# Optimization experiments

Measured on AMD Instinct MI355X. Metric: run time of the kernel, lower is better.

The kernel has to match this reference:

```python
import jax, jax.numpy as jnp
import numpy as np

N_USERS = 50000
N_ITEMS = 30000
N_ENTITIES = 100000
N_RELATIONS = 50
N_EDGES = 1500000
N_INTER = 1000000
D = 64
GAMMA = 0.1
MAX_ITER = 3


def _seg_sum(x, idx, n):
    return jax.ops.segment_sum(x, idx, num_segments=n)


def _seg_mean(x, idx, n):
    s = _seg_sum(x, idx, n)
    c = _seg_sum(jnp.ones((x.shape[0], 1), x.dtype), idx, n)
    return s / jnp.clip(c, 1.0)


def _masked_seg_mean(x, mask, idx, n):
    # scatter_mean over the subset of rows where mask is True (zeros for empty segments)
    w = mask.astype(x.dtype)[:, None]
    s = _seg_sum(x * w, idx, n)
    c = _seg_sum(w, idx, n)
    return s / jnp.clip(c, 1.0)


def _seg_softmax(p, idx, n):
    m = jax.ops.segment_max(p, idx, num_segments=n)
    e = jnp.exp(p - m[idx])
    z = _seg_sum(e, idx, n)
    return e / z[idx]


def _leaky_relu(x):
    return jnp.where(x >= 0, x, 0.01 * x)


def _normalize(x, eps=1e-12):
    n = jnp.linalg.norm(x, axis=1, keepdims=True)
    return x / jnp.maximum(n, eps)


def setup_inputs() -> dict:
    key = jax.random.key(0)
    ks = jax.random.split(key, 12)
    entity_emb = jax.random.normal(ks[0], (N_ENTITIES, D), jnp.float32) * 0.1
    user_emb = jax.random.normal(ks[1], (N_USERS, D), jnp.float32) * 0.1
    user_emb_cf = jax.random.normal(ks[2], (N_USERS, D), jnp.float32) * 0.1
    item_emb_cf = jax.random.normal(ks[3], (N_ITEMS, D), jnp.float32) * 0.1
    relation_weight = jax.random.normal(ks[4], (N_RELATIONS, D), jnp.float32) * 0.1
    edge_index = jax.random.randint(ks[5], (2, N_EDGES), 0, N_ENTITIES, jnp.int64 if jax.config.jax_enable_x64 else jnp.int32)
    edge_type = jax.random.randint(ks[6], (N_EDGES,), 0, N_RELATIONS, edge_index.dtype)
    rows = jax.random.randint(ks[7], (N_INTER, 1), 0, N_USERS, edge_index.dtype)
    cols = jax.random.randint(ks[8], (N_INTER, 1), 0, N_ITEMS, edge_index.dtype)
    interact_mat = jnp.concatenate([rows, cols], axis=1)
    W1_w = jax.random.normal(ks[9], (D, D), jnp.float32) * 0.1
    W1_b = jnp.zeros((D,), jnp.float32)
    W2_w = jax.random.normal(ks[10], (D, D), jnp.float32) * 0.1
    W2_b = jnp.zeros((D,), jnp.float32)
    return {
        "entity_emb": entity_emb, "user_emb": user_emb, "user_emb_cf": user_emb_cf,
        "item_emb_cf": item_emb_cf, "relation_weight": relation_weight,
        "W1_w": W1_w, "W1_b": W1_b, "W2_w": W2_w, "W2_b": W2_b,
        "edge_index": edge_index, "edge_type": edge_type, "interact_mat": interact_mat,
    }


def reference(entity_emb, user_emb, user_emb_cf, item_emb_cf, relation_weight,
              W1_w, W1_b, W2_w, W2_b, edge_index, edge_type, interact_mat):
    head, tail = edge_index[0], edge_index[1]
    cross = (head < N_ITEMS) ^ (tail < N_ITEMS)
    same = ~cross

    rel_emb = relation_weight[edge_type]          # [E, D]
    tail_emb = entity_emb[tail]                   # [E, D]

    agg1 = _masked_seg_mean(tail_emb * rel_emb, cross, head, N_ENTITIES)
    agg1 = _leaky_relu(agg1 @ W1_w.T + W1_b) / 2
    agg2 = _masked_seg_mean(tail_emb + rel_emb, same, head, N_ENTITIES)
    agg2 = _leaky_relu(agg2 @ W2_w.T + W2_b) / 2
    entity_agg = agg1 + agg2
    rel_ = _seg_mean(rel_emb, head, N_ENTITIES)   # [n_entities, D]

    mat_row = interact_mat[:, 0]
    mat_col = interact_mat[:, 1]
    item_emb_kg = entity_emb[:N_ITEMS]
    rel_i = rel_[:N_ITEMS]

    u, ucf, mask = None, None, None
    for i in range(MAX_ITER):
        ue = user_emb if u is None else u
        ucfe = user_emb_cf if ucf is None else ucf
        p = jax.nn.sigmoid(jnp.sum(ue[mat_row] * rel_i[mat_col] * item_emb_kg[mat_col], axis=1))
        pcf = jax.nn.sigmoid(jnp.sum(ucfe[mat_row] * item_emb_cf[mat_col], axis=1))
        p = _seg_softmax(p, mat_row, N_USERS)
        pcf = _seg_softmax(pcf, mat_row, N_USERS)
        mask = (jnp.abs(jax.nn.sigmoid(p) - jax.nn.sigmoid(pcf)) < GAMMA).astype(jnp.int32)[:, None]
        mf = mask.astype(p.dtype)
        u = _seg_sum(item_emb_kg[mat_col] * p[:, None] * mf, mat_row, N_USERS)
        ucf = _seg_sum(item_emb_cf[mat_col] * pcf[:, None] * mf, mat_row, N_USERS)
        if i < MAX_ITER - 1:
            u = _normalize(u)
            ucf = _normalize(ucf)

    item_agg = _seg_mean(user_emb_cf[mat_row], mat_col, N_ITEMS)
    return entity_agg, u, ucf, item_agg, mask
```

## Files before the change

kernel.cpp:

```cpp
#include <hip/hip_runtime.h>

#define NU 50000
#define NI 30000
#define NE 100000
#define NEDGE 1500000
#define NINTER 1000000
#define GAMMA 0.1f
#define CAP 192
#define KR 5
#define KSTG (4 * KR)
#define SB 1024

#define STRIPE_E 12500
#define STRIPE_R 6250
#define STRIPE_C 3750
#define SCATB 2048

__device__ __forceinline__ float frcp(float x) { return __builtin_amdgcn_rcpf(x); }
__device__ __forceinline__ float fsgm(float x) { return frcp(1.0f + __expf(-x)); }
__device__ __forceinline__ float dot4(float4 a, float4 b) {
  return a.x * b.x + a.y * b.y + a.z * b.z + a.w * b.w;
}
__device__ __forceinline__ int gidx(const void* p, long long i, int is64) {
  return is64 ? (int)((const long long*)p)[i] : ((const int*)p)[i];
}

__global__ void k_detect(const int* __restrict__ ei32, int* __restrict__ flag) {
  int all_zero = 1;
  for (int i = 1; i < 64; i += 2)
    if (ei32[i] != 0) { all_zero = 0; break; }
  *flag = all_zero;
}

__global__ __launch_bounds__(256) void k_hist(
    const void* __restrict__ ei, const void* __restrict__ im,
    int* __restrict__ cntE, int* __restrict__ cntR,
    int* __restrict__ cntC, const int* __restrict__ flagp) {
  int f = *flagp;
  int coh = blockIdx.x & 7;
  int ct = (blockIdx.x >> 3) * 256 + threadIdx.x;
  int cstride = (gridDim.x >> 3) * 256;
  int loE = coh * STRIPE_E, hiE = loE + STRIPE_E;
  int loR = coh * STRIPE_R, hiR = loR + STRIPE_R;
  int loC = coh * STRIPE_C, hiC = loC + STRIPE_C;
  for (int e = ct; e < NEDGE; e += cstride) {
    int h = gidx(ei, e, f);
    if (h >= loE && h < hiE) atomicAdd(&cntE[h], 1);
  }
  for (int t = ct; t < NINTER; t += cstride) {
    int r = gidx(im, 2LL * t, f);
    int c = gidx(im, 2LL * t + 1, f);
    if (r >= loR && r < hiR) atomicAdd(&cntR[r], 1);
    if (c >= loC && c < hiC) atomicAdd(&cntC[c], 1);
  }
}

__global__ void k_scan1(const int* __restrict__ in, int* __restrict__ out,
                        int* __restrict__ part, int n) {
  __shared__ int tmp[SB];
  int g = blockIdx.x * SB + threadIdx.x;
  int v = (g < n) ? in[g] : 0;
  tmp[threadIdx.x] = v; __syncthreads();
  for (int off = 1; off < SB; off <<= 1) {
    int t = (threadIdx.x >= off) ? tmp[threadIdx.x - off] : 0;
    __syncthreads();
    tmp[threadIdx.x] += t;
    __syncthreads();
  }
  if (g < n) out[g] = tmp[threadIdx.x] - v;
  if (threadIdx.x == SB - 1) part[blockIdx.x] = tmp[threadIdx.x];
}

__global__ void k_scan2(int* __restrict__ part, int nb) {
  __shared__ int tmp[SB];
  int v = (threadIdx.x < nb) ? part[threadIdx.x] : 0;
  tmp[threadIdx.x] = v; __syncthreads();
  for (int off = 1; off < SB; off <<= 1) {
    int t = (threadIdx.x >= off) ? tmp[threadIdx.x - off] : 0;
    __syncthreads();
    tmp[threadIdx.x] += t;
    __syncthreads();
  }
  if (threadIdx.x < nb) part[threadIdx.x] = tmp[threadIdx.x] - v;
}

__global__ void k_scan3(int* __restrict__ out, const int* __restrict__ part, int n) {
  int g = blockIdx.x * SB + threadIdx.x;
  if (g < n) out[g] += part[blockIdx.x];
}

__global__ __launch_bounds__(256) void k_scat(
    const void* __restrict__ ei, const void* __restrict__ et,
    const void* __restrict__ im,
    const int* __restrict__ startE, int* __restrict__ curE, int* __restrict__ SE,
    const int* __restrict__ startR, int* __restrict__ curR,
    int* __restrict__ SIcol, int* __restrict__ SIorig,
    const int* __restrict__ startC, int* __restrict__ curC,
    int* __restrict__ SCrow, const int* __restrict__ flagp) {
  int f = *flagp;
  int coh = blockIdx.x & 7;
  int ct = (blockIdx.x >> 3) * 256 + threadIdx.x;
  int cstride = (gridDim.x >> 3) * 256;
  int loE = coh * STRIPE_E, hiE = loE + STRIPE_E;
  int loR = coh * STRIPE_R, hiR = loR + STRIPE_R;
  int loC = coh * STRIPE_C, hiC = loC + STRIPE_C;
  for (int e = ct; e < NEDGE; e += cstride) {
    int h = gidx(ei, e, f);
    if (h >= loE && h < hiE) {
      int tl = gidx(ei, NEDGE + (long long)e, f), r = gidx(et, e, f);
      int pos = startE[h] + atomicAdd(&curE[h], 1);
      SE[pos] = tl | (r << 17);
    }
  }
  for (int t = ct; t < NINTER; t += cstride) {
    int r = gidx(im, 2LL * t, f);
    int c = gidx(im, 2LL * t + 1, f);
    if (r >= loR && r < hiR) {
      int pr = startR[r] + atomicAdd(&curR[r], 1);
      SIcol[pr] = c; SIorig[pr] = t;
    }
    if (c >= loC && c < hiC) {
      int pc = startC[c] + atomicAdd(&curC[c], 1);
      SCrow[pc] = r;
    }
  }
}

__global__ __launch_bounds__(256) void k_aggE(
    const int* __restrict__ SE, const int* __restrict__ startE, const int* __restrict__ cntE,
    const float* __restrict__ ent, const float* __restrict__ relw,
    const float* __restrict__ W1w, const float* __restrict__ W1b,
    const float* __restrict__ W2w, const float* __restrict__ W2b,
    float* __restrict__ out_entity, float* __restrict__ RIE) {
  __shared__ float w1[64 * 65], w2[64 * 65], b1[64], b2[64];
  __shared__ float xs1[4][64], xs2[4][64], xs3[4][64];
  int tid = threadIdx.x;
  for (int i = tid; i < 4096; i += 256) {
    w1[(i >> 6) * 65 + (i & 63)] = W1w[i];
    w2[(i >> 6) * 65 + (i & 63)] = W2w[i];
  }
  if (tid < 64) { b1[tid] = W1b[tid]; b2[tid] = W2b[tid]; }
  __syncthreads();
  int w = tid >> 6, lane = tid & 63;
  int g = lane >> 4, q = lane & 15;
  int h = blockIdx.x * 4 + w;
  if (h >= NE) return;
  int s = startE[h], n = cntE[h];
  bool hI = (h < NI);
  float4 a1 = {0, 0, 0, 0}, a2 = {0, 0, 0, 0}, rs = {0, 0, 0, 0};
  int c1 = 0;
  for (int i0 = 0; i0 < n; i0 += 4) {
    int i = i0 + g;
    bool act = i < n;
    if (act) {
      int v = SE[s + i];
      int tl = v & 0x1FFFF, rl = v >> 17;
      const float4 te = *(const float4*)&ent[tl * 64 + 4 * q];
      const float4 re = *(const float4*)&relw[rl * 64 + 4 * q];
      rs.x += re.x; rs.y += re.y; rs.z += re.z; rs.w += re.w;
      if (hI != (tl < NI)) {
        a1.x += te.x * re.x; a1.y += te.y * re.y;
        a1.z += te.z * re.z; a1.w += te.w * re.w;
        c1++;
      } else {
        a2.x += te.x + re.x; a2.y += te.y + re.y;
        a2.z += te.z + re.z; a2.w += te.w + re.w;
      }
    }
  }
#pragma unroll
  for (int off = 16; off <= 32; off <<= 1) {
    a1.x += __shfl_xor(a1.x, off, 64); a1.y += __shfl_xor(a1.y, off, 64);
    a1.z += __shfl_xor(a1.z, off, 64); a1.w += __shfl_xor(a1.w, off, 64);
    a2.x += __shfl_xor(a2.x, off, 64); a2.y += __shfl_xor(a2.y, off, 64);
    a2.z += __shfl_xor(a2.z, off, 64); a2.w += __shfl_xor(a2.w, off, 64);
    rs.x += __shfl_xor(rs.x, off, 64); rs.y += __shfl_xor(rs.y, off, 64);
    rs.z += __shfl_xor(rs.z, off, 64); rs.w += __shfl_xor(rs.w, off, 64);
    c1 += __shfl_xor(c1, off, 64);
  }
  int c2 = n - c1;
  float r1 = frcp((float)max(c1, 1)), r2 = frcp((float)max(c2, 1));
  float rn = frcp((float)max(n, 1));
  if (g == 0) {
    *(float4*)&xs1[w][4 * q] = make_float4(a1.x * r1, a1.y * r1, a1.z * r1, a1.w * r1);
    *(float4*)&xs2[w][4 * q] = make_float4(a2.x * r2, a2.y * r2, a2.z * r2, a2.w * r2);
    *(float4*)&xs3[w][4 * q] = make_float4(rs.x * rn, rs.y * rn, rs.z * rn, rs.w * rn);
  }
  __asm__ volatile("s_waitcnt lgkmcnt(0)");
  int d = lane;
  float acc1 = b1[d], acc2 = b2[d];
#pragma unroll 8
  for (int k = 0; k < 64; k++) {
    acc1 += xs1[w][k] * w1[d * 65 + k];
    acc2 += xs2[w][k] * w2[d * 65 + k];
  }
  acc1 = (acc1 >= 0.f ? acc1 : 0.01f * acc1) * 0.5f;
  acc2 = (acc2 >= 0.f ? acc2 : 0.01f * acc2) * 0.5f;
  out_entity[h * 64 + d] = acc1 + acc2;
  if (hI) RIE[h * 64 + d] = xs3[w][d] * ent[h * 64 + d];
}

__global__ __launch_bounds__(256, 4) void k_phaseB(
    const int* __restrict__ SIcol, const int* __restrict__ SIorig,
    const int* __restrict__ startR, const int* __restrict__ cntR,
    const float* __restrict__ ue, const float* __restrict__ uce,
    const float* __restrict__ RIE, const float* __restrict__ ent,
    const float* __restrict__ icf,
    float* __restrict__ out_u, float* __restrict__ out_ucf,
    float* __restrict__ out_mask) {
  __shared__ float eP[4][CAP + 4], ePC[4][CAP + 4];
  __shared__ int cols[4][CAP + 4];
  int tid = threadIdx.x, w = tid >> 6, lane = tid & 63;
  int g = lane >> 4, q = lane & 15;
  int r = blockIdx.x * 4 + w;
  if (r >= NU) return;
  int s = startR[r], n = cntR[r];
  if (n > CAP) n = CAP;
  for (int i = lane; i < n; i += 64) cols[w][i] = SIcol[s + i];
  __asm__ volatile("s_waitcnt lgkmcnt(0) vmcnt(0)");
  float4 u4  = *(const float4*)&ue[r * 64 + 4 * q];
  float4 uc4 = *(const float4*)&uce[r * 64 + 4 * q];

  float4 rieS[KR], icfS[KR], entS[KR];
#pragma unroll
  for (int kk = 0; kk < KR; kk++) {
    int i = 4 * kk + g;
    rieS[kk] = make_float4(0, 0, 0, 0);
    icfS[kk] = make_float4(0, 0, 0, 0);
    entS[kk] = make_float4(0, 0, 0, 0);
    if (i < n) {
      int c = cols[w][i];
      rieS[kk] = *(const float4*)&RIE[c * 64 + 4 * q];
      icfS[kk] = *(const float4*)&icf[c * 64 + 4 * q];
      entS[kk] = *(const float4*)&ent[c * 64 + 4 * q];
    }
  }

  for (int it = 0; it < 3; it++) {
    float Zp = 0.f, ZCp = 0.f;
    float epS[KR], epcS[KR];
#pragma unroll
    for (int kk = 0; kk < KR; kk++) {
      int i = 4 * kk + g;
      bool act = i < n;
      float v1 = 0.f, v2 = 0.f;
      if (act) {
        v1 = dot4(u4,  rieS[kk]);
        v2 = dot4(uc4, icfS[kk]);
      }
#pragma unroll
      for (int off = 1; off <= 8; off <<= 1) {
        v1 += __shfl_xor(v1, off, 64);
        v2 += __shfl_xor(v2, off, 64);
      }
      float ep = __expf(fsgm(v1)), epc = __expf(fsgm(v2));
      epS[kk] = ep; epcS[kk] = epc;
      if (act) { Zp += ep; ZCp += epc; }
    }
    for (int i0 = KSTG; i0 < n; i0 += 4) {
      int i = i0 + g;
      bool act = i < n;
      float v1 = 0.f, v2 = 0.f;
      if (act) {
        int c = cols[w][i];
        v1 = dot4(u4,  *(const float4*)&RIE[c * 64 + 4 * q]);
        v2 = dot4(uc4, *(const float4*)&icf[c * 64 + 4 * q]);
      }
#pragma unroll
      for (int off = 1; off <= 8; off <<= 1) {
        v1 += __shfl_xor(v1, off, 64);
        v2 += __shfl_xor(v2, off, 64);
      }
      float ep = __expf(fsgm(v1)), epc = __expf(fsgm(v2));
      if (act) {
        if (q == 0) { eP[w][i] = ep; ePC[w][i] = epc; }
        Zp += ep; ZCp += epc;
      }
    }
    float Zs = Zp, ZCs = ZCp;
#pragma unroll
    for (int off = 16; off <= 32; off <<= 1) {
      Zs += __shfl_xor(Zs, off, 64);
      ZCs += __shfl_xor(ZCs, off, 64);
    }
    __asm__ volatile("s_waitcnt lgkmcnt(0)");
    float rz = frcp(Zs), rzc = frcp(ZCs);
    float4 ua = {0, 0, 0, 0}, uca = {0, 0, 0, 0};
#pragma unroll
    for (int kk = 0; kk < KR; kk++) {
      int i = 4 * kk + g;
      if (i < n) {
        float p = epS[kk] * rz, pc = epcS[kk] * rzc;
        bool m = fabsf(fsgm(p) - fsgm(pc)) < GAMMA;
        if (it == 2 && q == 0) out_mask[SIorig[s + i]] = m ? 1.0f : 0.0f;
        if (m) {
          ua.x += entS[kk].x * p; ua.y += entS[kk].y * p;
          ua.z += entS[kk].z * p; ua.w += entS[kk].w * p;
          uca.x += icfS[kk].x * pc; uca.y += icfS[kk].y * pc;
          uca.z += icfS[kk].z * pc; uca.w += icfS[kk].w * pc;
        }
      }
    }
    for (int i0 = KSTG; i0 < n; i0 += 4) {
      int i = i0 + g;
      if (i < n) {
        int c = cols[w][i];
        float p = eP[w][i] * rz, pc = ePC[w][i] * rzc;
        bool m = fabsf(fsgm(p) - fsgm(pc)) < GAMMA;
        if (it == 2 && q == 0) out_mask[SIorig[s + i]] = m ? 1.0f : 0.0f;
        if (m) {
          const float4 e4 = *(const float4*)&ent[c * 64 + 4 * q];
          const float4 i4 = *(const float4*)&icf[c * 64 + 4 * q];
          ua.x += e4.x * p; ua.y += e4.y * p; ua.z += e4.z * p; ua.w += e4.w * p;
          uca.x += i4.x * pc; uca.y += i4.y * pc; uca.z += i4.z * pc; uca.w += i4.w * pc;
        }
      }
    }
#pragma unroll
    for (int off = 16; off <= 32; off <<= 1) {
      ua.x += __shfl_xor(ua.x, off, 64); ua.y += __shfl_xor(ua.y, off, 64);
      ua.z += __shfl_xor(ua.z, off, 64); ua.w += __shfl_xor(ua.w, off, 64);
      uca.x += __shfl_xor(uca.x, off, 64); uca.y += __shfl_xor(uca.y, off, 64);
      uca.z += __shfl_xor(uca.z, off, 64); uca.w += __shfl_xor(uca.w, off, 64);
    }
    if (it < 2) {
      float s1 = dot4(ua, ua), s2 = dot4(uca, uca);
#pragma unroll
      for (int off = 1; off <= 8; off <<= 1) {
        s1 += __shfl_xor(s1, off, 64);
        s2 += __shfl_xor(s2, off, 64);
      }
      float k1 = frcp(fmaxf(sqrtf(s1), 1e-12f)), k2 = frcp(fmaxf(sqrtf(s2), 1e-12f));
      ua.x *= k1; ua.y *= k1; ua.z *= k1; ua.w *= k1;
      uca.x *= k2; uca.y *= k2; uca.z *= k2; uca.w *= k2;
    }
    u4 = ua; uc4 = uca;
  }
  if (g == 0) {
    *(float4*)&out_u[r * 64 + 4 * q] = u4;
    *(float4*)&out_ucf[r * 64 + 4 * q] = uc4;
  }
}

__global__ __launch_bounds__(256) void k_itemA(
    const int* __restrict__ SCrow, const int* __restrict__ startC,
    const int* __restrict__ cntC, const float* __restrict__ ucf,
    float* __restrict__ out_item) {
  int tid = threadIdx.x, w = tid >> 6, lane = tid & 63;
  int g = lane >> 4, q = lane & 15;
  int c = blockIdx.x * 4 + w;
  if (c >= NI) return;
  int s = startC[c], n = cntC[c];
  float4 a = {0, 0, 0, 0};
  for (int i0 = 0; i0 < n; i0 += 4) {
    int i = i0 + g;
    if (i < n) {
      const float4 v = *(const float4*)&ucf[SCrow[s + i] * 64 + 4 * q];
      a.x += v.x; a.y += v.y; a.z += v.z; a.w += v.w;
    }
  }
#pragma unroll
  for (int off = 16; off <= 32; off <<= 1) {
    a.x += __shfl_xor(a.x, off, 64); a.y += __shfl_xor(a.y, off, 64);
    a.z += __shfl_xor(a.z, off, 64); a.w += __shfl_xor(a.w, off, 64);
  }
  float rn = frcp((float)max(n, 1));
  if (g == 0) {
    *(float4*)&out_item[c * 64 + 4 * q] =
        make_float4(a.x * rn, a.y * rn, a.z * rn, a.w * rn);
  }
}

static void scan(int* cnt, int* start, int* part, int n, hipStream_t st) {
  int nb = (n + SB - 1) / SB;
  k_scan1<<<nb, SB, 0, st>>>(cnt, start, part, n);
  k_scan2<<<1, SB, 0, st>>>(part, nb);
  k_scan3<<<nb, SB, 0, st>>>(start, part, n);
}

extern "C" void kernel_launch(void* const* d_in, const int* in_sizes, int n_in,
                              void* d_out, int out_size, void* d_ws, size_t ws_size,
                              hipStream_t stream) {
  const float* entity_emb  = (const float*)d_in[0];
  const float* user_emb    = (const float*)d_in[1];
  const float* user_emb_cf = (const float*)d_in[2];
  const float* item_emb_cf = (const float*)d_in[3];
  const float* relw        = (const float*)d_in[4];
  const float* W1w = (const float*)d_in[5];
  const float* W1b = (const float*)d_in[6];
  const float* W2w = (const float*)d_in[7];
  const float* W2b = (const float*)d_in[8];
  const void* edge_index   = d_in[9];
  const void* edge_type    = d_in[10];
  const void* interact_mat = d_in[11];

  float* out = (float*)d_out;
  float* out_entity = out;
  float* out_u      = out + 6400000;
  float* out_ucf    = out + 9600000;
  float* out_item   = out + 12800000;
  float* out_mask   = out + 14720000;

  float* W = (float*)d_ws;
  int*   SE     = (int*)W;
  int*   SIcol  = (int*)(W + 3000000);
  int*   SIorig = (int*)(W + 4000000);
  int*   SCrow  = (int*)(W + 5000000);
  float* RIE    = W + 6000000;
  int*   cntE   = (int*)(W + 7920000);
  int*   startE = (int*)(W + 8020000);
  int*   curE   = (int*)(W + 8120000);
  int*   cntR   = (int*)(W + 8220000);
  int*   startR = (int*)(W + 8270000);
  int*   curR   = (int*)(W + 8320000);
  int*   cntC   = (int*)(W + 8370000);
  int*   startC = (int*)(W + 8400000);
  int*   curC   = (int*)(W + 8430000);
  int*   part   = (int*)(W + 8460000);
  int*   FL     = (int*)(W + 8462048);

  k_detect<<<1, 1, 0, stream>>>((const int*)edge_index, FL);
  hipMemsetAsync(cntE, 0, (size_t)(8462048 - 7920000) * 4, stream);

  k_hist<<<SCATB, 256, 0, stream>>>(edge_index, interact_mat, cntE, cntR, cntC, FL);
  scan(cntE, startE, part, NE, stream);
  scan(cntR, startR, part, NU, stream);
  scan(cntC, startC, part, NI, stream);
  k_scat<<<SCATB, 256, 0, stream>>>(edge_index, edge_type, interact_mat,
                                    startE, curE, SE,
                                    startR, curR, SIcol, SIorig,
                                    startC, curC, SCrow, FL);

  k_aggE<<<(NE + 3) / 4, 256, 0, stream>>>(SE, startE, cntE, entity_emb, relw,
                                           W1w, W1b, W2w, W2b, out_entity, RIE);
  k_phaseB<<<(NU + 3) / 4, 256, 0, stream>>>(SIcol, SIorig, startR, cntR,
                                             user_emb, user_emb_cf, RIE,
                                             entity_emb, item_emb_cf,
                                             out_u, out_ucf, out_mask);
  k_itemA<<<(NI + 3) / 4, 256, 0, stream>>>(SCrow, startC, cntC, user_emb_cf, out_item);
}
```

Measured before the change: 900.8 us.

## Merge scans, pretranspose MLP weights, use DPP reductions, raise phaseB occupancy

Several independent changes. The three CSR prefix scans become one scan over a concatenated count array, with per-segment bias subtraction, which cuts kernel launches. k_aggE drops its per-block shared-memory weight staging and reads pre-transposed weights from global/L2 so consecutive lanes read coalesced addresses. k_phaseB swaps shfl_xor reductions for DPP row reductions, keeps entity rows and exp scores in LDS rather than registers, and raises launch bounds to 8 waves per SIMD, trading more LDS per block for lower register pressure.

```diff
diff --git a/kernel.cpp b/kernel.cpp
--- a/kernel.cpp
+++ b/kernel.cpp
@@ -10,6 +10,7 @@
 #define KR 5
 #define KSTG (4 * KR)
 #define SB 1024
+#define NSCAN 180000
 
 #define STRIPE_E 12500
 #define STRIPE_R 6250
@@ -23,6 +24,14 @@
 }
 __device__ __forceinline__ int gidx(const void* p, long long i, int is64) {
   return is64 ? (int)((const long long*)p)[i] : ((const int*)p)[i];
+}
+
+__device__ __forceinline__ float red16(float v) {
+  v += __int_as_float(__builtin_amdgcn_update_dpp(0, __float_as_int(v), 0xB1, 0xF, 0xF, true));
+  v += __int_as_float(__builtin_amdgcn_update_dpp(0, __float_as_int(v), 0x4E, 0xF, 0xF, true));
+  v += __int_as_float(__builtin_amdgcn_update_dpp(0, __float_as_int(v), 0x141, 0xF, 0xF, true));
+  v += __int_as_float(__builtin_amdgcn_update_dpp(0, __float_as_int(v), 0x140, 0xF, 0xF, true));
+  return v;
 }
 
 __global__ void k_detect(const int* __restrict__ ei32, int* __restrict__ flag) {
@@ -30,6 +39,16 @@
   for (int i = 1; i < 64; i += 2)
     if (ei32[i] != 0) { all_zero = 0; break; }
   *flag = all_zero;
+}
+
+__global__ void k_wt(const float* __restrict__ W1w, const float* __restrict__ W2w,
+                     float* __restrict__ WT1, float* __restrict__ WT2) {
+  int i = blockIdx.x * 256 + threadIdx.x;
+  if (i < 4096) {
+    int r = i >> 6, c = i & 63;
+    WT1[c * 64 + r] = W1w[i];
+    WT2[c * 64 + r] = W2w[i];
+  }
 }
 
 __global__ __launch_bounds__(256) void k_hist(
@@ -86,7 +105,10 @@
 
 __global__ void k_scan3(int* __restrict__ out, const int* __restrict__ part, int n) {
   int g = blockIdx.x * SB + threadIdx.x;
-  if (g < n) out[g] += part[blockIdx.x];
+  if (g < n) {
+    int bias = (g >= 150000) ? (NEDGE + NINTER) : ((g >= 100000) ? NEDGE : 0);
+    out[g] += part[blockIdx.x] - bias;
+  }
 }
 
 __global__ __launch_bounds__(256) void k_scat(
@@ -129,18 +151,11 @@
 __global__ __launch_bounds__(256) void k_aggE(
     const int* __restrict__ SE, const int* __restrict__ startE, const int* __restrict__ cntE,
     const float* __restrict__ ent, const float* __restrict__ relw,
-    const float* __restrict__ W1w, const float* __restrict__ W1b,
-    const float* __restrict__ W2w, const float* __restrict__ W2b,
+    const float* __restrict__ WT1, const float* __restrict__ W1b,
+    const float* __restrict__ WT2, const float* __restrict__ W2b,
     float* __restrict__ out_entity, float* __restrict__ RIE) {
-  __shared__ float w1[64 * 65], w2[64 * 65], b1[64], b2[64];
   __shared__ float xs1[4][64], xs2[4][64], xs3[4][64];
   int tid = threadIdx.x;
-  for (int i = tid; i < 4096; i += 256) {
-    w1[(i >> 6) * 65 + (i & 63)] = W1w[i];
-    w2[(i >> 6) * 65 + (i & 63)] = W2w[i];
-  }
-  if (tid < 64) { b1[tid] = W1b[tid]; b2[tid] = W2b[tid]; }
-  __syncthreads();
   int w = tid >> 6, lane = tid & 63;
   int g = lane >> 4, q = lane & 15;
   int h = blockIdx.x * 4 + w;
@@ -188,11 +203,11 @@
   }
   __asm__ volatile("s_waitcnt lgkmcnt(0)");
   int d = lane;
-  float acc1 = b1[d], acc2 = b2[d];
+  float acc1 = W1b[d], acc2 = W2b[d];
 #pragma unroll 8
   for (int k = 0; k < 64; k++) {
-    acc1 += xs1[w][k] * w1[d * 65 + k];
-    acc2 += xs2[w][k] * w2[d * 65 + k];
+    acc1 += xs1[w][k] * WT1[k * 64 + d];
+    acc2 += xs2[w][k] * WT2[k * 64 + d];
   }
   acc1 = (acc1 >= 0.f ? acc1 : 0.01f * acc1) * 0.5f;
   acc2 = (acc2 >= 0.f ? acc2 : 0.01f * acc2) * 0.5f;
@@ -200,7 +215,7 @@
   if (hI) RIE[h * 64 + d] = xs3[w][d] * ent[h * 64 + d];
 }
 
-__global__ __launch_bounds__(256, 4) void k_phaseB(
+__global__ __launch_bounds__(256, 8) void k_phaseB(
     const int* __restrict__ SIcol, const int* __restrict__ SIorig,
     const int* __restrict__ startR, const int* __restrict__ cntR,
     const float* __restrict__ ue, const float* __restrict__ uce,
@@ -210,6 +225,7 @@
     float* __restrict__ out_mask) {
   __shared__ float eP[4][CAP + 4], ePC[4][CAP + 4];
   __shared__ int cols[4][CAP + 4];
+  __shared__ float entL[4][KSTG][68];
   int tid = threadIdx.x, w = tid >> 6, lane = tid & 63;
   int g = lane >> 4, q = lane & 15;
   int r = blockIdx.x * 4 + w;
@@ -221,24 +237,22 @@
   float4 u4  = *(const float4*)&ue[r * 64 + 4 * q];
   float4 uc4 = *(const float4*)&uce[r * 64 + 4 * q];
 
-  float4 rieS[KR], icfS[KR], entS[KR];
+  float4 rieS[KR], icfS[KR];
 #pragma unroll
   for (int kk = 0; kk < KR; kk++) {
     int i = 4 * kk + g;
     rieS[kk] = make_float4(0, 0, 0, 0);
     icfS[kk] = make_float4(0, 0, 0, 0);
-    entS[kk] = make_float4(0, 0, 0, 0);
     if (i < n) {
       int c = cols[w][i];
       rieS[kk] = *(const float4*)&RIE[c * 64 + 4 * q];
       icfS[kk] = *(const float4*)&icf[c * 64 + 4 * q];
-      entS[kk] = *(const float4*)&ent[c * 64 + 4 * q];
+      *(float4*)&entL[w][i][4 * q] = *(const float4*)&ent[c * 64 + 4 * q];
     }
   }
 
   for (int it = 0; it < 3; it++) {
     float Zp = 0.f, ZCp = 0.f;
-    float epS[KR], epcS[KR];
 #pragma unroll
     for (int kk = 0; kk < KR; kk++) {
       int i = 4 * kk + g;
@@ -248,14 +262,12 @@
         v1 = dot4(u4,  rieS[kk]);
         v2 = dot4(uc4, icfS[kk]);
       }
-#pragma unroll
-      for (int off = 1; off <= 8; off <<= 1) {
-        v1 += __shfl_xor(v1, off, 64);
-        v2 += __shfl_xor(v2, off, 64);
-      }
+      v1 = red16(v1); v2 = red16(v2);
       float ep = __expf(fsgm(v1)), epc = __expf(fsgm(v2));
-      epS[kk] = ep; epcS[kk] = epc;
-      if (act) { Zp += ep; ZCp += epc; }
+      if (act) {
+        if (q == 0) { eP[w][i] = ep; ePC[w][i] = epc; }
+        Zp += ep; ZCp += epc;
+      }
     }
     for (int i0 = KSTG; i0 < n; i0 += 4) {
       int i = i0 + g;
@@ -266,11 +278,7 @@
         v1 = dot4(u4,  *(const float4*)&RIE[c * 64 + 4 * q]);
         v2 = dot4(uc4, *(const float4*)&icf[c * 64 + 4 * q]);
       }
-#pragma unroll
-      for (int off = 1; off <= 8; off <<= 1) {
-        v1 += __shfl_xor(v1, off, 64);
-        v2 += __shfl_xor(v2, off, 64);
-      }
+      v1 = red16(v1); v2 = red16(v2);
       float ep = __expf(fsgm(v1)), epc = __expf(fsgm(v2));
       if (act) {
         if (q == 0) { eP[w][i] = ep; ePC[w][i] = epc; }
@@ -290,12 +298,12 @@
     for (int kk = 0; kk < KR; kk++) {
       int i = 4 * kk + g;
       if (i < n) {
-        float p = epS[kk] * rz, pc = epcS[kk] * rzc;
+        float p = eP[w][i] * rz, pc = ePC[w][i] * rzc;
         bool m = fabsf(fsgm(p) - fsgm(pc)) < GAMMA;
         if (it == 2 && q == 0) out_mask[SIorig[s + i]] = m ? 1.0f : 0.0f;
         if (m) {
-          ua.x += entS[kk].x * p; ua.y += entS[kk].y * p;
-          ua.z += entS[kk].z * p; ua.w += entS[kk].w * p;
+          const float4 e4 = *(const float4*)&entL[w][i][4 * q];
+          ua.x += e4.x * p; ua.y += e4.y * p; ua.z += e4.z * p; ua.w += e4.w * p;
           uca.x += icfS[kk].x * pc; uca.y += icfS[kk].y * pc;
           uca.z += icfS[kk].z * pc; uca.w += icfS[kk].w * pc;
         }
@@ -324,12 +332,8 @@
       uca.z += __shfl_xor(uca.z, off, 64); uca.w += __shfl_xor(uca.w, off, 64);
     }
     if (it < 2) {
-      float s1 = dot4(ua, ua), s2 = dot4(uca, uca);
-#pragma unroll
-      for (int off = 1; off <= 8; off <<= 1) {
-        s1 += __shfl_xor(s1, off, 64);
-        s2 += __shfl_xor(s2, off, 64);
-      }
+      float s1 = red16(dot4(ua, ua));
+      float s2 = red16(dot4(uca, uca));
       float k1 = frcp(fmaxf(sqrtf(s1), 1e-12f)), k2 = frcp(fmaxf(sqrtf(s2), 1e-12f));
       ua.x *= k1; ua.y *= k1; ua.z *= k1; ua.w *= k1;
       uca.x *= k2; uca.y *= k2; uca.z *= k2; uca.w *= k2;
@@ -371,13 +375,6 @@
   }
 }
 
-static void scan(int* cnt, int* start, int* part, int n, hipStream_t st) {
-  int nb = (n + SB - 1) / SB;
-  k_scan1<<<nb, SB, 0, st>>>(cnt, start, part, n);
-  k_scan2<<<1, SB, 0, st>>>(part, nb);
-  k_scan3<<<nb, SB, 0, st>>>(start, part, n);
-}
-
 extern "C" void kernel_launch(void* const* d_in, const int* in_sizes, int n_in,
                               void* d_out, int out_size, void* d_ws, size_t ws_size,
                               hipStream_t stream) {
@@ -403,36 +400,40 @@
 
   float* W = (float*)d_ws;
   int*   SE     = (int*)W;
+  float* WT1    = W + 1500000;
+  float* WT2    = W + 1504096;
   int*   SIcol  = (int*)(W + 3000000);
   int*   SIorig = (int*)(W + 4000000);
   int*   SCrow  = (int*)(W + 5000000);
   float* RIE    = W + 6000000;
-  int*   cntE   = (int*)(W + 7920000);
-  int*   startE = (int*)(W + 8020000);
-  int*   curE   = (int*)(W + 8120000);
-  int*   cntR   = (int*)(W + 8220000);
-  int*   startR = (int*)(W + 8270000);
-  int*   curR   = (int*)(W + 8320000);
-  int*   cntC   = (int*)(W + 8370000);
-  int*   startC = (int*)(W + 8400000);
-  int*   curC   = (int*)(W + 8430000);
+  int*   cntALL = (int*)(W + 7920000);
+  int*   curALL = (int*)(W + 8100000);
+  int*   startALL = (int*)(W + 8280000);
   int*   part   = (int*)(W + 8460000);
   int*   FL     = (int*)(W + 8462048);
 
+  int* cntE = cntALL;            int* cntR = cntALL + 100000;   int* cntC = cntALL + 150000;
+  int* curE = curALL;            int* curR = curALL + 100000;   int* curC = curALL + 150000;
+  int* startE = startALL;        int* startR = startALL + 100000; int* startC = startALL + 150000;
+
   k_detect<<<1, 1, 0, stream>>>((const int*)edge_index, FL);
-  hipMemsetAsync(cntE, 0, (size_t)(8462048 - 7920000) * 4, stream);
+  k_wt<<<16, 256, 0, stream>>>(W1w, W2w, WT1, WT2);
+  hipMemsetAsync(cntALL, 0, (size_t)360000 * 4, stream);
 
   k_hist<<<SCATB, 256, 0, stream>>>(edge_index, interact_mat, cntE, cntR, cntC, FL);
-  scan(cntE, startE, part, NE, stream);
-  scan(cntR, startR, part, NU, stream);
-  scan(cntC, startC, part, NI, stream);
+  {
+    int nb = (NSCAN + SB - 1) / SB;
+    k_scan1<<<nb, SB, 0, stream>>>(cntALL, startALL, part, NSCAN);
+    k_scan2<<<1, SB, 0, stream>>>(part, nb);
+    k_scan3<<<nb, SB, 0, stream>>>(startALL, part, NSCAN);
+  }
   k_scat<<<SCATB, 256, 0, stream>>>(edge_index, edge_type, interact_mat,
                                     startE, curE, SE,
                                     startR, curR, SIcol, SIorig,
                                     startC, curC, SCrow, FL);
 
   k_aggE<<<(NE + 3) / 4, 256, 0, stream>>>(SE, startE, cntE, entity_emb, relw,
-                                           W1w, W1b, W2w, W2b, out_entity, RIE);
+                                           WT1, W1b, WT2, W2b, out_entity, RIE);
   k_phaseB<<<(NU + 3) / 4, 256, 0, stream>>>(SIcol, SIorig, startR, cntR,
                                              user_emb, user_emb_cf, RIE,
                                              entity_emb, item_emb_cf,
```

After: 822.1 us. -8.7%, faster.
